# Kernel tuning notes

Measured on AMD Instinct MI355X. Metric: run time of the kernel, lower is better.

## Reference

```python
import jax, jax.numpy as jnp
import numpy as np
from jax import lax

B, L, H, I, Z = 1024, 128, 256, 32, 128  # batch, max_length, hidden, input_size, latent


def setup_inputs() -> dict:
    key = jax.random.key(0)
    ks = jax.random.split(key, 32)
    p = lambda k, shape: (jax.random.normal(k, shape, dtype=jnp.float32) * 0.05)
    d = {
        "x": jax.random.normal(ks[0], (B, Z), dtype=jnp.float32),
        "W1": p(ks[1], (512, Z)), "b1": p(ks[2], (512,)),
        "W2": p(ks[3], (512, 512)), "b2": p(ks[4], (512,)),
        "W3": p(ks[5], (512, 512)), "b3": p(ks[6], (512,)),
        # predict_h / predict_c / predict_x_0 heads
        "Wh1": p(ks[7], (512, 512)), "bh1": p(ks[8], (512,)),
        "Wh2": p(ks[9], (H, 512)), "bh2": p(ks[10], (H,)),
        "Wc1": p(ks[11], (512, 512)), "bc1": p(ks[12], (512,)),
        "Wc2": p(ks[13], (H, 512)), "bc2": p(ks[14], (H,)),
        "Wx1": p(ks[15], (512, 512)), "bx1": p(ks[16], (512,)),
        "Wx2": p(ks[17], (H, 512)), "bx2": p(ks[18], (H,)),
        # decode LSTM (input H -> hidden H), PyTorch gate order i,f,g,o
        "rWih": p(ks[19], (4 * H, H)), "rWhh": p(ks[20], (4 * H, H)),
        "rbih": p(ks[21], (4 * H,)), "rbhh": p(ks[22], (4 * H,)),
        # predictor LSTM (input H -> hidden I)
        "pWih": p(ks[23], (4 * I, H)), "pWhh": p(ks[24], (4 * I, I)),
        "pbih": p(ks[25], (4 * I,)), "pbhh": p(ks[26], (4 * I,)),
    }
    return d


def _leaky(v):
    return jnp.where(v >= 0, v, 0.2 * v)


def _lstm_cell(xt, h, c, Wih, Whh, b):
    gates = xt @ Wih.T + h @ Whh.T + b  # [B, 4G]
    i, f, g, o = jnp.split(gates, 4, axis=-1)
    c_new = jax.nn.sigmoid(f) * c + jax.nn.sigmoid(i) * jnp.tanh(g)
    h_new = jax.nn.sigmoid(o) * jnp.tanh(c_new)
    return h_new, c_new


def _forward(x, W1, b1, W2, b2, W3, b3, Wh1, bh1, Wh2, bh2, Wc1, bc1, Wc2, bc2,
             Wx1, bx1, Wx2, bx2, rWih, rWhh, rbih, rbhh, pWih, pWhh, pbih, pbhh):
    t = _leaky(x @ W1.T + b1)
    t = _leaky(t @ W2.T + b2)
    t = _leaky(t @ W3.T + b3)
    h = _leaky(t @ Wh1.T + bh1) @ Wh2.T + bh2   # [B, H]
    c = _leaky(t @ Wc1.T + bc1) @ Wc2.T + bc2   # [B, H]
    x0 = _leaky(t @ Wx1.T + bx1) @ Wx2.T + bx2  # [B, H]

    rb = rbih + rbhh
    # The torch loop re-feeds the growing sequence through the LSTM from the
    # same initial (h, c) each step; deterministically this equals a single
    # O(L) self-feeding scan: token_{i} = h-output of step i, fed at step i+1.
    def dec_step(carry, _):
        tok, hh, cc = carry
        h2, c2 = _lstm_cell(tok, hh, cc, rWih, rWhh, rb)
        return (h2, h2, c2), h2

    _, outs = lax.scan(dec_step, (x0, h, c), None, length=L)  # [L, B, H]

    pb = pbih + pbhh
    def pred_step(carry, xt):
        hh, cc = carry
        hh, cc = _lstm_cell(xt, hh, cc, pWih, pWhh, pb)
        return (hh, cc), hh

    h0 = jnp.zeros((B, I), dtype=x.dtype)
    _, pouts = lax.scan(pred_step, (h0, h0), outs)  # [L, B, I]
    y = jnp.transpose(pouts, (1, 0, 2))  # [B, L, I]

    layer_type = jax.nn.softmax(y[..., : I - 1], axis=-1)
    features = jax.nn.sigmoid(y[..., I - 1:])
    return jnp.concatenate([layer_type, features], axis=-1)


def reference(x, W1, b1, W2, b2, W3, b3, Wh1, bh1, Wh2, bh2, Wc1, bc1, Wc2, bc2,
              Wx1, bx1, Wx2, bx2, rWih, rWhh, rbih, rbhh, pWih, pWhh, pbih, pbhh):
    return _forward(x, W1, b1, W2, b2, W3, b3, Wh1, bh1, Wh2, bh2, Wc1, bc1, Wc2, bc2,
                    Wx1, bx1, Wx2, bx2, rWih, rWhh, rbih, rbhh, pWih, pWhh, pbih, pbhh)
```

## Files before the change

kernel.cpp:

```cpp
#include <hip/hip_runtime.h>
#include <hip/hip_fp8.h>

typedef unsigned short u16;
typedef unsigned char u8;
typedef __attribute__((ext_vector_type(8))) __bf16 bfrag;
typedef long long f8frag;
typedef __attribute__((ext_vector_type(4))) float f32x4;

static __device__ __forceinline__ f32x4 MFMA(bfrag a, bfrag b, f32x4 c) {
  return __builtin_amdgcn_mfma_f32_16x16x32_bf16(a, b, c, 0, 0, 0);
}
static __device__ __forceinline__ f32x4 MFMA8(f8frag a, f8frag b, f32x4 c) {
  return __builtin_amdgcn_mfma_f32_16x16x32_fp8_fp8(a, b, c, 0, 0, 0);
}

static __device__ __forceinline__ u16 f2b(float f) {
  union { float f; unsigned u; } v; v.f = f;
  unsigned r = (v.u + 0x7fffu + ((v.u >> 16) & 1u)) >> 16;
  return (u16)r;
}
static __device__ __forceinline__ u8 f2e4m3(float f) {
  return (u8)(__builtin_amdgcn_cvt_pk_fp8_f32(f, f, 0, false) & 0xff);
}
static __device__ __forceinline__ unsigned pk4_e4m3(float a, float b, float c, float d) {
  int p = __builtin_amdgcn_cvt_pk_fp8_f32(a, b, 0, false);
  p = __builtin_amdgcn_cvt_pk_fp8_f32(c, d, p, true);
  return (unsigned)p;
}
static __device__ __forceinline__ float rcp(float x) { return __builtin_amdgcn_rcpf(x); }
static __device__ __forceinline__ float ssig(float x) {
  float E = __expf(x);
  return E * rcp(1.f + E);
}
static __device__ __forceinline__ float stanh(float x) {
  float E = __expf(2.f * x);
  return 1.f - 2.f * rcp(E + 1.f);
}
static __device__ __forceinline__ float2 lstm2(float gi, float gf, float gg,
                                               float go, float c) {
  float Ei = __expf(gi), Ef = __expf(gf), Eg = __expf(2.f * gg), Eo = __expf(go);
  float P = 1.f + Ef, Q = 1.f + Ei, R = 1.f + Eg;
  float QR = Q * R;
  float num = c * Ef * QR + Ei * P * (Eg - 1.f);
  float cn = num * rcp(P * QR);
  float Ec = __expf(2.f * cn);
  float hn = Eo * (Ec - 1.f) * rcp((1.f + Eo) * (Ec + 1.f));
  return make_float2(hn, cn);
}

#define LDS_BARRIER() asm volatile("s_waitcnt lgkmcnt(0)\ns_barrier" ::: "memory")
#define PIN_A8(A) asm volatile("" : "+a"(A[0]), "+a"(A[1]), "+a"(A[2]), "+a"(A[3]), \
                                    "+a"(A[4]), "+a"(A[5]), "+a"(A[6]), "+a"(A[7]))
#define PIN_V8(A) asm volatile("" : "+v"(A[0]), "+v"(A[1]), "+v"(A[2]), "+v"(A[3]), \
                                    "+v"(A[4]), "+v"(A[5]), "+v"(A[6]), "+v"(A[7]))

struct PrepArgs {
  const float *x, *W1, *W2, *W3, *Wh1, *Wc1, *Wx1, *Wh2, *Wc2, *Wx2;
  const float *rWih, *rWhh, *rbih, *rbhh, *pWih, *pWhh, *pbih, *pbhh;
  u16 *Xbf, *W1b, *W2b, *W3b, *Wh1b, *Wc1b, *Wx1b, *Wh2b, *Wc2b, *Wx2b;
  u16 *WcatR;
  u8 *WsS, *pWsS, *pWhhS;
  float *rbR, *pbR;
};

static __device__ __forceinline__ void emit_stream(u16* dst, const float* src,
                                                   int i, int K, int ktbits) {
  int j = i & 7, lane = (i >> 3) & 63;
  int kt = (i >> 9) & ((1 << ktbits) - 1);
  int nt = (i >> (9 + ktbits)) & 3;
  int ct = i >> (11 + ktbits);
  int srow = ct * 64 + nt * 16 + (lane & 15);
  int scol = kt * 32 + ((lane >> 4) & 3) * 8 + j;
  dst[i] = f2b(src[srow * K + scol]);
}

__global__ __launch_bounds__(256) void prep(PrepArgs p) {
  const int tid0 = blockIdx.x * 256 + threadIdx.x;
  const int stride = gridDim.x * 256;
  switch (blockIdx.y) {
    case 0: for (int i = tid0; i < 131072; i += stride) p.Xbf[i] = f2b(p.x[i]); break;
    case 1: for (int i = tid0; i < 65536;  i += stride) emit_stream(p.W1b, p.W1, i, 128, 2); break;
    case 2: for (int i = tid0; i < 262144; i += stride) emit_stream(p.W2b, p.W2, i, 512, 4); break;
    case 3: for (int i = tid0; i < 262144; i += stride) emit_stream(p.W3b, p.W3, i, 512, 4); break;
    case 4: for (int i = tid0; i < 262144; i += stride) emit_stream(p.Wh1b, p.Wh1, i, 512, 4); break;
    case 5: for (int i = tid0; i < 262144; i += stride) emit_stream(p.Wc1b, p.Wc1, i, 512, 4); break;
    case 6: for (int i = tid0; i < 262144; i += stride) emit_stream(p.Wx1b, p.Wx1, i, 512, 4); break;
    case 7: for (int i = tid0; i < 131072; i += stride) emit_stream(p.Wh2b, p.Wh2, i, 512, 4); break;
    case 8: for (int i = tid0; i < 131072; i += stride) emit_stream(p.Wc2b, p.Wc2, i, 512, 4); break;
    case 9: for (int i = tid0; i < 131072; i += stride) emit_stream(p.Wx2b, p.Wx2, i, 512, 4); break;
    case 10:
      for (int i = tid0; i < 262144; i += stride) {
        int n = i >> 8, k = i & 255;
        int srow = (((n >> 4) & 3) << 8) + ((n >> 6) << 4) + (n & 15);
        p.WcatR[n * 512 + k] = f2b(p.rWih[srow * 256 + k]);
        p.WcatR[n * 512 + 256 + k] = f2b(p.rWhh[srow * 256 + k]);
      }
      break;
    case 11:
      for (int i = tid0; i < 1024; i += stride) {
        int srow = (((i >> 4) & 3) << 8) + ((i >> 6) << 4) + (i & 15);
        p.rbR[i] = p.rbih[srow] + p.rbhh[srow];
      }
      break;
    case 12:
      for (int i = tid0; i < 32768; i += stride) {
        int j = i & 7, lane = (i >> 3) & 63, kt = (i >> 9) & 7, w = i >> 12;
        int n = w * 16 + (lane & 15);
        int srow = ((n & 3) << 5) + (n >> 2);
        int k = kt * 32 + ((lane >> 4) & 3) * 8 + j;
        p.pWsS[i] = f2e4m3(p.pWih[srow * 256 + k]);
      }
      break;
    case 13:
      for (int i = tid0; i < 4096; i += stride) {
        int j = i & 7, lane = (i >> 3) & 63, w = i >> 9;
        int n = w * 16 + (lane & 15);
        int srow = ((n & 3) << 5) + (n >> 2);
        int k = ((lane >> 4) & 3) * 8 + j;
        p.pWhhS[i] = f2e4m3(p.pWhh[srow * 32 + k]);
      }
      break;
    case 14:
      for (int i = tid0; i < 128; i += stride) {
        int srow = ((i & 3) << 5) + (i >> 2);
        p.pbR[i] = p.pbih[srow] + p.pbhh[srow];
      }
      break;
    case 15:
      for (int i = tid0; i < 262144; i += stride) {
        int j = i & 7, lane = (i >> 3) & 63, kt = (i >> 9) & 7;
        int gate = (i >> 12) & 3, g16 = i >> 14;
        int srow = gate * 256 + g16 * 16 + (lane & 15);
        int k = kt * 32 + ((lane >> 4) & 3) * 8 + j;
        p.WsS[i] = f2e4m3(p.rWih[srow * 256 + k] + p.rWhh[srow * 256 + k]);
      }
      break;
  }
}

__global__ __launch_bounds__(256) void gemm_act(
    const u16* __restrict__ X, const u16* __restrict__ W,
    const float* __restrict__ bias,
    u16* __restrict__ Yb, float* __restrict__ Yf,
    int K, int ldo, int coloff, int leaky) {
  const int rt = blockIdx.x, ct = blockIdx.y;
  const int lane = threadIdx.x & 63, wave = threadIdx.x >> 6;
  const int m15 = lane & 15, q = lane >> 4, kq = q * 8;
  const int KT = K >> 5;
  const int row = rt * 64 + wave * 16 + m15;
  f32x4 acc[4] = {};
  const u16* xp = X + (size_t)row * K + kq;
  const u16* wst = W + lane * 8;
  for (int kt = 0; kt < KT; kt++) {
    bfrag a = *(const bfrag*)(xp + kt * 32);
#pragma unroll
    for (int nt = 0; nt < 4; nt++) {
      const u16* wp = wst + (size_t)((ct * 4 + nt) * KT + kt) * 512;
      acc[nt] = MFMA(a, *(const bfrag*)wp, acc[nt]);
    }
  }
#pragma unroll
  for (int nt = 0; nt < 4; nt++) {
    int col = ct * 64 + nt * 16 + m15;
    float bv = bias[col];
#pragma unroll
    for (int r = 0; r < 4; r++) {
      int orow = rt * 64 + wave * 16 + q * 4 + r;
      float v = acc[nt][r] + bv;
      if (leaky) v = v >= 0.f ? v : 0.2f * v;
      if (Yb) Yb[(size_t)orow * ldo + coloff + col] = f2b(v);
      else    Yf[(size_t)orow * ldo + coloff + col] = v;
    }
  }
}

__global__ __launch_bounds__(256) void decode_step(
    const u16* __restrict__ A, const u16* __restrict__ W,
    const float* __restrict__ rb,
    float* __restrict__ C, u16* __restrict__ Hout, int K) {
  __shared__ float g[64][128];
  const int rt = blockIdx.x, cg = blockIdx.y;
  const int lane = threadIdx.x & 63, wave = threadIdx.x >> 6;
  const int m15 = lane & 15, q = lane >> 4, kq = q * 8;
  const int row = rt * 64 + wave * 16 + m15;
  f32x4 acc[8] = {};
  const u16* ap = A + (size_t)row * K + kq;
  for (int k0 = 0; k0 < K; k0 += 32) {
    bfrag a = *(const bfrag*)(ap + k0);
#pragma unroll
    for (int nt = 0; nt < 8; nt++) {
      const u16* wp = W + (size_t)(cg * 128 + nt * 16 + m15) * K + k0 + kq;
      acc[nt] = MFMA(a, *(const bfrag*)wp, acc[nt]);
    }
  }
#pragma unroll
  for (int nt = 0; nt < 8; nt++)
#pragma unroll
    for (int r = 0; r < 4; r++)
      g[wave * 16 + q * 4 + r][nt * 16 + m15] = acc[nt][r];
  __syncthreads();
  for (int t = threadIdx.x; t < 2048; t += 256) {
    int rl = t >> 5, hc = t & 31;
    int grow = rt * 64 + rl, gcol = cg * 32 + hc;
    int base = ((hc >> 4) << 6) + (hc & 15);
    float gi = g[rl][base +  0] + rb[cg * 128 + base +  0];
    float gf = g[rl][base + 16] + rb[cg * 128 + base + 16];
    float gg = g[rl][base + 32] + rb[cg * 128 + base + 32];
    float go = g[rl][base + 48] + rb[cg * 128 + base + 48];
    size_t ci = (size_t)grow * 256 + gcol;
    float c = C[ci];
    float2 hc2 = lstm2(gi, gf, gg, go, c);
    C[ci] = hc2.y;
    Hout[ci] = f2b(hc2.x);
  }
}

__global__ __attribute__((amdgpu_flat_work_group_size(1024, 1024), amdgpu_waves_per_eu(4, 4)))
void decode_h(
    const u8* __restrict__ WsS,
    const float* __restrict__ rb,
    const float* __restrict__ C0,
    const u16* __restrict__ H0,
    u8* __restrict__ hG) {
  __shared__ __align__(16) u8 hbufS[2][4096];
  __shared__ __align__(16) u8 WoL[16][4096];
  const int tid = threadIdx.x;
  const int w = tid >> 6, lane = tid & 63;
  const int m15 = lane & 15, q = lane >> 4;
  const int b = blockIdx.x;
  const int rowg = b * 16;

  {
    int4* dst = (int4*)WoL;
    for (int i = tid; i < 4096; i += 1024) {
      int wv = i >> 8, rest = i & 255;
      dst[i] = ((const int4*)(WsS + wv * 16384 + 12288))[rest];
    }
  }
  {
    int r = tid >> 6, c = (tid & 63) * 4;
    const u16* src = H0 + (size_t)(rowg + r) * 256 + c;
    float f0, f1, f2, f3;
    { union { float f; unsigned u; } v; v.u = (unsigned)src[0] << 16; f0 = v.f; }
    { union { float f; unsigned u; } v; v.u = (unsigned)src[1] << 16; f1 = v.f; }
    { union { float f; unsigned u; } v; v.u = (unsigned)src[2] << 16; f2 = v.f; }
    { union { float f; unsigned u; } v; v.u = (unsigned)src[3] << 16; f3 = v.f; }
    unsigned hv = pk4_e4m3(f0, f1, f2, f3);
    int off = (c >> 5) * 512 + ((c >> 3) & 3) * 128 + r * 8 + (c & 4);
    *(unsigned*)(&hbufS[0][off]) = hv;
    *(unsigned*)(hG + (size_t)b * 524288 + off) = hv;
  }
  f32x4 cst = *(const f32x4*)(C0 + (size_t)(rowg + m15) * 256 + w * 16 + q * 4);
  const float* rbp = rb + w * 64 + q * 4;
  f32x4 rbv0 = *(const f32x4*)(rbp +  0);
  f32x4 rbv1 = *(const f32x4*)(rbp + 16);
  f32x4 rbv2 = *(const f32x4*)(rbp + 32);
  f32x4 rbv3 = *(const f32x4*)(rbp + 48);
  asm volatile("" : "+v"(rbv0), "+v"(rbv1), "+v"(rbv2), "+v"(rbv3));
  const u8* wsb = WsS + (size_t)w * 16384 + lane * 8;
  f8frag Wv0[8], Wv1[8], Wv2[8];
#pragma unroll
  for (int kt = 0; kt < 8; kt++) {
    Wv0[kt] = *(const f8frag*)(wsb + kt * 512);
    Wv1[kt] = *(const f8frag*)(wsb + 4096 + kt * 512);
    Wv2[kt] = *(const f8frag*)(wsb + 8192 + kt * 512);
  }
  PIN_A8(Wv0); PIN_A8(Wv1); PIN_A8(Wv2);
  const int wroff = (w >> 1) * 512 + ((w & 1) * 2 + (q >> 1)) * 128 + m15 * 8 + (q & 1) * 4;
  const u8* woW = &WoL[w][lane * 8];
  u8* hGs = hG + (size_t)b * 524288 + wroff;
  __syncthreads();

  for (int s = 1; s < 128; s++) {
    PIN_A8(Wv0); PIN_A8(Wv1); PIN_A8(Wv2);
    asm volatile("" : "+v"(rbv0), "+v"(rbv1), "+v"(rbv2), "+v"(rbv3));
    const u8* h8 = &hbufS[(s - 1) & 1][lane * 8];
    f32x4 ai = rbv0, af_ = rbv1, ag = rbv2, ao = rbv3;
#pragma unroll
    for (int kt = 0; kt < 8; kt++) {
      f8frag a8 = *(const f8frag*)(h8 + kt * 512);
      f8frag wo = *(const f8frag*)(woW + kt * 512);
      ai  = MFMA8(Wv0[kt], a8, ai);
      af_ = MFMA8(Wv1[kt], a8, af_);
      ag  = MFMA8(Wv2[kt], a8, ag);
      ao  = MFMA8(wo, a8, ao);
    }
    float hn[4];
#pragma unroll
    for (int r = 0; r < 4; r++) {
      float2 hc2 = lstm2(ai[r], af_[r], ag[r], ao[r], cst[r]);
      hn[r] = hc2.x;
      cst[r] = hc2.y;
    }
    unsigned hv = pk4_e4m3(hn[0], hn[1], hn[2], hn[3]);
    *(unsigned*)(&hbufS[s & 1][wroff]) = hv;
    *(unsigned*)(hGs + s * 4096) = hv;
    LDS_BARRIER();
  }
}

__global__ __launch_bounds__(512, 2) void pred_y(
    const u8* __restrict__ hG,
    const u8* __restrict__ pWsS,
    const u8* __restrict__ pWhhS,
    const float* __restrict__ pb,
    float* __restrict__ out) {
  __shared__ __align__(16) u8 stageL[16384];
  __shared__ __align__(16) u8 hp8[2][16][40];
  __shared__ float ysC[4][16][36];
  const int tid = threadIdx.x;
  const int w = tid >> 6, lane = tid & 63;
  const int m15 = lane & 15, q = lane >> 4;
  const int b = blockIdx.x, rowg = b * 16;
  for (int i = tid; i < 2 * 16 * 40; i += 512) (&hp8[0][0][0])[i] = 0;
  const u8* pwsb = pWsS + (size_t)w * 4096 + lane * 8;
  f8frag pbv[8];
#pragma unroll
  for (int kt = 0; kt < 8; kt++) pbv[kt] = *(const f8frag*)(pwsb + kt * 512);
  f8frag phw = *(const f8frag*)(pWhhS + (size_t)w * 512 + lane * 8);
  PIN_V8(pbv);
  asm volatile("" : "+v"(phw));
  const f32x4 pbias = *(const f32x4*)(pb + w * 16 + q * 4);
  float cp = 0.f;
  const int4* hGb = (const int4*)(hG + (size_t)b * 524288);
  const int t_si = (tid >> 3) >> 4, t_r = (tid >> 3) & 15, sub = tid & 7;
  __syncthreads();

  for (int cs = 0; cs < 32; cs++) {
    {
      int4* sdst = (int4*)stageL;
      sdst[tid] = hGb[cs * 1024 + tid];
      sdst[tid + 512] = hGb[cs * 1024 + tid + 512];
    }
    __syncthreads();
#pragma unroll
    for (int si = 0; si < 4; si++) {
      const int s = cs * 4 + si;
      const u8* xr8 = &stageL[si * 4096 + lane * 8];
      f32x4 pacc = pbias;
#pragma unroll
      for (int kt = 0; kt < 8; kt++) {
        f8frag pav = *(const f8frag*)(xr8 + kt * 512);
        pacc = MFMA8(pbv[kt], pav, pacc);
      }
      f8frag pah = *(const f8frag*)(&hp8[s & 1][m15][q * 8]);
      pacc = MFMA8(phw, pah, pacc);
      float2 hc2 = lstm2(pacc[0], pacc[1], pacc[2], pacc[3], cp);
      cp = hc2.y;
      hp8[(s + 1) & 1][m15][w * 4 + q] = f2e4m3(hc2.x);
      ysC[si][m15][w * 4 + q] = hc2.x;
      LDS_BARRIER();
    }
    {
      f32x4 yv = *(const f32x4*)&ysC[t_si][t_r][sub * 4];
      float v3 = (sub == 7) ? -1e30f : yv[3];
      float m = fmaxf(fmaxf(yv[0], yv[1]), fmaxf(yv[2], v3));
#pragma unroll
      for (int off = 4; off; off >>= 1) m = fmaxf(m, __shfl_xor(m, off, 8));
      float e0 = __expf(yv[0] - m), e1 = __expf(yv[1] - m), e2 = __expf(yv[2] - m);
      float e3 = (sub == 7) ? 0.f : __expf(yv[3] - m);
      float tot = e0 + e1 + e2 + e3;
#pragma unroll
      for (int off = 4; off; off >>= 1) tot += __shfl_xor(tot, off, 8);
      float inv = rcp(tot);
      f32x4 o;
      o[0] = e0 * inv; o[1] = e1 * inv; o[2] = e2 * inv;
      o[3] = (sub == 7) ? ssig(yv[3]) : e3 * inv;
      *(f32x4*)(out + (size_t)(rowg + t_r) * 4096 + (cs * 4 + t_si) * 32 + sub * 4) = o;
    }
    LDS_BARRIER();
  }
}

extern "C" void kernel_launch(void* const* d_in, const int* in_sizes, int n_in,
                              void* d_out, int out_size, void* d_ws, size_t ws_size,
                              hipStream_t stream) {
  (void)in_sizes; (void)n_in; (void)out_size; (void)ws_size;
  const float* x    = (const float*)d_in[0];
  const float* W1   = (const float*)d_in[1];
  const float* b1   = (const float*)d_in[2];
  const float* W2   = (const float*)d_in[3];
  const float* b2   = (const float*)d_in[4];
  const float* W3   = (const float*)d_in[5];
  const float* b3   = (const float*)d_in[6];
  const float* Wh1  = (const float*)d_in[7];
  const float* bh1  = (const float*)d_in[8];
  const float* Wh2  = (const float*)d_in[9];
  const float* bh2  = (const float*)d_in[10];
  const float* Wc1  = (const float*)d_in[11];
  const float* bc1  = (const float*)d_in[12];
  const float* Wc2  = (const float*)d_in[13];
  const float* bc2  = (const float*)d_in[14];
  const float* Wx1  = (const float*)d_in[15];
  const float* bx1  = (const float*)d_in[16];
  const float* Wx2  = (const float*)d_in[17];
  const float* bx2  = (const float*)d_in[18];
  const float* rWih = (const float*)d_in[19];
  const float* rWhh = (const float*)d_in[20];
  const float* rbih = (const float*)d_in[21];
  const float* rbhh = (const float*)d_in[22];
  const float* pWih = (const float*)d_in[23];
  const float* pWhh = (const float*)d_in[24];
  const float* pbih = (const float*)d_in[25];
  const float* pbhh = (const float*)d_in[26];

  char* w = (char*)d_ws;
  auto alloc = [&](size_t bytes) -> char* {
    char* p = w;
    w += (bytes + 255) & ~(size_t)255;
    return p;
  };
  u16* Xbf  = (u16*)alloc(1024 * 128 * 2);
  u16* T1   = (u16*)alloc(1024 * 512 * 2);
  u16* T2   = (u16*)alloc(1024 * 512 * 2);
  u16* T3   = (u16*)alloc(1024 * 512 * 2);
  u16* TH   = (u16*)alloc(1024 * 512 * 2);
  u16* TC   = (u16*)alloc(1024 * 512 * 2);
  u16* TX   = (u16*)alloc(1024 * 512 * 2);
  u16* X0H  = (u16*)alloc(1024 * 512 * 2);
  float* CB = (float*)alloc(1024 * 256 * 4);
  u16* OUTS0= (u16*)alloc(1024 * 256 * 2);
  u16* W1b  = (u16*)alloc(512 * 128 * 2);
  u16* W2b  = (u16*)alloc(512 * 512 * 2);
  u16* W3b  = (u16*)alloc(512 * 512 * 2);
  u16* Wh1b = (u16*)alloc(512 * 512 * 2);
  u16* Wc1b = (u16*)alloc(512 * 512 * 2);
  u16* Wx1b = (u16*)alloc(512 * 512 * 2);
  u16* Wh2b = (u16*)alloc(256 * 512 * 2);
  u16* Wc2b = (u16*)alloc(256 * 512 * 2);
  u16* Wx2b = (u16*)alloc(256 * 512 * 2);
  u16* WcatR= (u16*)alloc(1024 * 512 * 2);
  u8*  WsS  = (u8*)alloc(262144);
  u8*  pWsS = (u8*)alloc(32768);
  u8*  pWhhS= (u8*)alloc(4096);
  float* rbR = (float*)alloc(1024 * 4);
  float* pbR = (float*)alloc(128 * 4);
  u8*  hG   = (u8*)alloc((size_t)64 * 128 * 4096);

  PrepArgs pa;
  pa.x = x; pa.W1 = W1; pa.W2 = W2; pa.W3 = W3; pa.Wh1 = Wh1; pa.Wc1 = Wc1; pa.Wx1 = Wx1;
  pa.Wh2 = Wh2; pa.Wc2 = Wc2; pa.Wx2 = Wx2;
  pa.rWih = rWih; pa.rWhh = rWhh; pa.rbih = rbih; pa.rbhh = rbhh;
  pa.pWih = pWih; pa.pWhh = pWhh; pa.pbih = pbih; pa.pbhh = pbhh;
  pa.Xbf = Xbf; pa.W1b = W1b; pa.W2b = W2b; pa.W3b = W3b; pa.Wh1b = Wh1b;
  pa.Wc1b = Wc1b; pa.Wx1b = Wx1b; pa.Wh2b = Wh2b; pa.Wc2b = Wc2b; pa.Wx2b = Wx2b;
  pa.WcatR = WcatR;
  pa.WsS = WsS; pa.pWsS = pWsS; pa.pWhhS = pWhhS;
  pa.rbR = rbR; pa.pbR = pbR;
  prep<<<dim3(32, 16), 256, 0, stream>>>(pa);

  gemm_act<<<dim3(16, 8), 256, 0, stream>>>(Xbf, W1b, b1, T1, nullptr, 128, 512, 0, 1);
  gemm_act<<<dim3(16, 8), 256, 0, stream>>>(T1, W2b, b2, T2, nullptr, 512, 512, 0, 1);
  gemm_act<<<dim3(16, 8), 256, 0, stream>>>(T2, W3b, b3, T3, nullptr, 512, 512, 0, 1);
  gemm_act<<<dim3(16, 8), 256, 0, stream>>>(T3, Wh1b, bh1, TH, nullptr, 512, 512, 0, 1);
  gemm_act<<<dim3(16, 8), 256, 0, stream>>>(T3, Wc1b, bc1, TC, nullptr, 512, 512, 0, 1);
  gemm_act<<<dim3(16, 8), 256, 0, stream>>>(T3, Wx1b, bx1, TX, nullptr, 512, 512, 0, 1);
  gemm_act<<<dim3(16, 4), 256, 0, stream>>>(TH, Wh2b, bh2, X0H, nullptr, 512, 512, 256, 0);
  gemm_act<<<dim3(16, 4), 256, 0, stream>>>(TC, Wc2b, bc2, nullptr, CB, 512, 256, 0, 0);
  gemm_act<<<dim3(16, 4), 256, 0, stream>>>(TX, Wx2b, bx2, X0H, nullptr, 512, 512, 0, 0);

  decode_step<<<dim3(16, 8), 256, 0, stream>>>(X0H, WcatR, rbR, CB, OUTS0, 512);
  decode_h<<<64, 1024, 0, stream>>>(WsS, rbR, CB, OUTS0, hG);
  pred_y<<<64, 512, 0, stream>>>(hG, pWsS, pWhhS, pbR, (float*)d_out);
}
```

Measured before the change: 517.8 us.

## Fold first decode LSTM step into decode_h and batch head GEMMs into grouped launches

Removes the separate decode_step kernel by computing the first LSTM step (bf16 MFMA over the concatenated input/hidden weights, re-laid out in MFMA fragment order) inside decode_h, eliminating the OUTS0 round-trip and one launch. The three head GEMMs of each layer are merged into single grouped launches via blockIdx.z, cutting launch count from six to two. In exchange, each decode_h block now streams its slice of the 1 MB WcatR weights from global memory before the recurrent loop, which adds startup latency to a 64-block kernel.

```diff
diff --git a/kernel.cpp b/kernel.cpp
--- a/kernel.cpp
+++ b/kernel.cpp
@@ -31,10 +31,6 @@
 static __device__ __forceinline__ float ssig(float x) {
   float E = __expf(x);
   return E * rcp(1.f + E);
-}
-static __device__ __forceinline__ float stanh(float x) {
-  float E = __expf(2.f * x);
-  return 1.f - 2.f * rcp(E + 1.f);
 }
 static __device__ __forceinline__ float2 lstm2(float gi, float gf, float gg,
                                                float go, float c) {
@@ -89,11 +85,13 @@
     case 8: for (int i = tid0; i < 131072; i += stride) emit_stream(p.Wc2b, p.Wc2, i, 512, 4); break;
     case 9: for (int i = tid0; i < 131072; i += stride) emit_stream(p.Wx2b, p.Wx2, i, 512, 4); break;
     case 10:
-      for (int i = tid0; i < 262144; i += stride) {
-        int n = i >> 8, k = i & 255;
-        int srow = (((n >> 4) & 3) << 8) + ((n >> 6) << 4) + (n & 15);
-        p.WcatR[n * 512 + k] = f2b(p.rWih[srow * 256 + k]);
-        p.WcatR[n * 512 + 256 + k] = f2b(p.rWhh[srow * 256 + k]);
+      for (int i = tid0; i < 524288; i += stride) {
+        int j = i & 7, lane = (i >> 3) & 63, kt = (i >> 9) & 15;
+        int gate = (i >> 13) & 3, w16 = i >> 15;
+        int srow = gate * 256 + w16 * 16 + (lane & 15);
+        int k = kt * 32 + ((lane >> 4) & 3) * 8 + j;
+        float v = (k < 256) ? p.rWih[srow * 256 + k] : p.rWhh[srow * 256 + (k - 256)];
+        p.WcatR[i] = f2b(v);
       }
       break;
     case 11:
@@ -174,53 +172,53 @@
   }
 }
 
-__global__ __launch_bounds__(256) void decode_step(
-    const u16* __restrict__ A, const u16* __restrict__ W,
-    const float* __restrict__ rb,
-    float* __restrict__ C, u16* __restrict__ Hout, int K) {
-  __shared__ float g[64][128];
-  const int rt = blockIdx.x, cg = blockIdx.y;
+struct G3 {
+  const u16 *X, *W;
+  const float* bias;
+  u16* Yb;
+  float* Yf;
+  int K, ldo, coloff, leaky;
+};
+__global__ __launch_bounds__(256) void gemm_act3(G3 ga, G3 gb, G3 gc) {
+  G3 g = (blockIdx.z == 0) ? ga : (blockIdx.z == 1) ? gb : gc;
+  const int rt = blockIdx.x, ct = blockIdx.y;
   const int lane = threadIdx.x & 63, wave = threadIdx.x >> 6;
   const int m15 = lane & 15, q = lane >> 4, kq = q * 8;
+  const int KT = g.K >> 5;
   const int row = rt * 64 + wave * 16 + m15;
-  f32x4 acc[8] = {};
-  const u16* ap = A + (size_t)row * K + kq;
-  for (int k0 = 0; k0 < K; k0 += 32) {
-    bfrag a = *(const bfrag*)(ap + k0);
-#pragma unroll
-    for (int nt = 0; nt < 8; nt++) {
-      const u16* wp = W + (size_t)(cg * 128 + nt * 16 + m15) * K + k0 + kq;
+  f32x4 acc[4] = {};
+  const u16* xp = g.X + (size_t)row * g.K + kq;
+  const u16* wst = g.W + lane * 8;
+  for (int kt = 0; kt < KT; kt++) {
+    bfrag a = *(const bfrag*)(xp + kt * 32);
+#pragma unroll
+    for (int nt = 0; nt < 4; nt++) {
+      const u16* wp = wst + (size_t)((ct * 4 + nt) * KT + kt) * 512;
       acc[nt] = MFMA(a, *(const bfrag*)wp, acc[nt]);
     }
   }
 #pragma unroll
-  for (int nt = 0; nt < 8; nt++)
-#pragma unroll
-    for (int r = 0; r < 4; r++)
-      g[wave * 16 + q * 4 + r][nt * 16 + m15] = acc[nt][r];
-  __syncthreads();
-  for (int t = threadIdx.x; t < 2048; t += 256) {
-    int rl = t >> 5, hc = t & 31;
-    int grow = rt * 64 + rl, gcol = cg * 32 + hc;
-    int base = ((hc >> 4) << 6) + (hc & 15);
-    float gi = g[rl][base +  0] + rb[cg * 128 + base +  0];
-    float gf = g[rl][base + 16] + rb[cg * 128 + base + 16];
-    float gg = g[rl][base + 32] + rb[cg * 128 + base + 32];
-    float go = g[rl][base + 48] + rb[cg * 128 + base + 48];
-    size_t ci = (size_t)grow * 256 + gcol;
-    float c = C[ci];
-    float2 hc2 = lstm2(gi, gf, gg, go, c);
-    C[ci] = hc2.y;
-    Hout[ci] = f2b(hc2.x);
+  for (int nt = 0; nt < 4; nt++) {
+    int col = ct * 64 + nt * 16 + m15;
+    float bv = g.bias[col];
+#pragma unroll
+    for (int r = 0; r < 4; r++) {
+      int orow = rt * 64 + wave * 16 + q * 4 + r;
+      float v = acc[nt][r] + bv;
+      if (g.leaky) v = v >= 0.f ? v : 0.2f * v;
+      if (g.Yb) g.Yb[(size_t)orow * g.ldo + g.coloff + col] = f2b(v);
+      else      g.Yf[(size_t)orow * g.ldo + g.coloff + col] = v;
+    }
   }
 }
 
 __global__ __attribute__((amdgpu_flat_work_group_size(1024, 1024), amdgpu_waves_per_eu(4, 4)))
 void decode_h(
     const u8* __restrict__ WsS,
+    const u16* __restrict__ WcatR,
     const float* __restrict__ rb,
-    const float* __restrict__ C0,
-    const u16* __restrict__ H0,
+    const float* __restrict__ CB,
+    const u16* __restrict__ X0H,
     u8* __restrict__ hG) {
   __shared__ __align__(16) u8 hbufS[2][4096];
   __shared__ __align__(16) u8 WoL[16][4096];
@@ -237,26 +235,39 @@
       dst[i] = ((const int4*)(WsS + wv * 16384 + 12288))[rest];
     }
   }
-  {
-    int r = tid >> 6, c = (tid & 63) * 4;
-    const u16* src = H0 + (size_t)(rowg + r) * 256 + c;
-    float f0, f1, f2, f3;
-    { union { float f; unsigned u; } v; v.u = (unsigned)src[0] << 16; f0 = v.f; }
-    { union { float f; unsigned u; } v; v.u = (unsigned)src[1] << 16; f1 = v.f; }
-    { union { float f; unsigned u; } v; v.u = (unsigned)src[2] << 16; f2 = v.f; }
-    { union { float f; unsigned u; } v; v.u = (unsigned)src[3] << 16; f3 = v.f; }
-    unsigned hv = pk4_e4m3(f0, f1, f2, f3);
-    int off = (c >> 5) * 512 + ((c >> 3) & 3) * 128 + r * 8 + (c & 4);
-    *(unsigned*)(&hbufS[0][off]) = hv;
-    *(unsigned*)(hG + (size_t)b * 524288 + off) = hv;
-  }
-  f32x4 cst = *(const f32x4*)(C0 + (size_t)(rowg + m15) * 256 + w * 16 + q * 4);
   const float* rbp = rb + w * 64 + q * 4;
   f32x4 rbv0 = *(const f32x4*)(rbp +  0);
   f32x4 rbv1 = *(const f32x4*)(rbp + 16);
   f32x4 rbv2 = *(const f32x4*)(rbp + 32);
   f32x4 rbv3 = *(const f32x4*)(rbp + 48);
   asm volatile("" : "+v"(rbv0), "+v"(rbv1), "+v"(rbv2), "+v"(rbv3));
+  f32x4 cst = *(const f32x4*)(CB + (size_t)(rowg + m15) * 256 + w * 16 + q * 4);
+  const int wroff = (w >> 1) * 512 + ((w & 1) * 2 + (q >> 1)) * 128 + m15 * 8 + (q & 1) * 4;
+  u8* hGs = hG + (size_t)b * 524288 + wroff;
+
+  {
+    f32x4 ai = rbv0, af_ = rbv1, ag = rbv2, ao = rbv3;
+    const u16* xrow = X0H + (size_t)(rowg + m15) * 512 + q * 8;
+    const u16* wcw = WcatR + (size_t)w * 32768 + lane * 8;
+#pragma unroll
+    for (int kt = 0; kt < 16; kt++) {
+      bfrag a = *(const bfrag*)(xrow + kt * 32);
+      ai  = MFMA(*(const bfrag*)(wcw + kt * 512), a, ai);
+      af_ = MFMA(*(const bfrag*)(wcw + 8192 + kt * 512), a, af_);
+      ag  = MFMA(*(const bfrag*)(wcw + 16384 + kt * 512), a, ag);
+      ao  = MFMA(*(const bfrag*)(wcw + 24576 + kt * 512), a, ao);
+    }
+    float hn[4];
+#pragma unroll
+    for (int r = 0; r < 4; r++) {
+      float2 hc2 = lstm2(ai[r], af_[r], ag[r], ao[r], cst[r]);
+      hn[r] = hc2.x;
+      cst[r] = hc2.y;
+    }
+    unsigned hv = pk4_e4m3(hn[0], hn[1], hn[2], hn[3]);
+    *(unsigned*)(&hbufS[0][wroff]) = hv;
+    *(unsigned*)hGs = hv;
+  }
   const u8* wsb = WsS + (size_t)w * 16384 + lane * 8;
   f8frag Wv0[8], Wv1[8], Wv2[8];
 #pragma unroll
@@ -266,9 +277,7 @@
     Wv2[kt] = *(const f8frag*)(wsb + 8192 + kt * 512);
   }
   PIN_A8(Wv0); PIN_A8(Wv1); PIN_A8(Wv2);
-  const int wroff = (w >> 1) * 512 + ((w & 1) * 2 + (q >> 1)) * 128 + m15 * 8 + (q & 1) * 4;
   const u8* woW = &WoL[w][lane * 8];
-  u8* hGs = hG + (size_t)b * 524288 + wroff;
   __syncthreads();
 
   for (int s = 1; s < 128; s++) {
@@ -294,7 +303,7 @@
     }
     unsigned hv = pk4_e4m3(hn[0], hn[1], hn[2], hn[3]);
     *(unsigned*)(&hbufS[s & 1][wroff]) = hv;
-    *(unsigned*)(hGs + s * 4096) = hv;
+    *(unsigned*)(hGs + (size_t)s * 4096) = hv;
     LDS_BARRIER();
   }
 }
@@ -419,7 +428,6 @@
   u16* TX   = (u16*)alloc(1024 * 512 * 2);
   u16* X0H  = (u16*)alloc(1024 * 512 * 2);
   float* CB = (float*)alloc(1024 * 256 * 4);
-  u16* OUTS0= (u16*)alloc(1024 * 256 * 2);
   u16* W1b  = (u16*)alloc(512 * 128 * 2);
   u16* W2b  = (u16*)alloc(512 * 512 * 2);
   u16* W3b  = (u16*)alloc(512 * 512 * 2);
@@ -452,14 +460,15 @@
   gemm_act<<<dim3(16, 8), 256, 0, stream>>>(Xbf, W1b, b1, T1, nullptr, 128, 512, 0, 1);
   gemm_act<<<dim3(16, 8), 256, 0, stream>>>(T1, W2b, b2, T2, nullptr, 512, 512, 0, 1);
   gemm_act<<<dim3(16, 8), 256, 0, stream>>>(T2, W3b, b3, T3, nullptr, 512, 512, 0, 1);
-  gemm_act<<<dim3(16, 8), 256, 0, stream>>>(T3, Wh1b, bh1, TH, nullptr, 512, 512, 0, 1);
-  gemm_act<<<dim3(16, 8), 256, 0, stream>>>(T3, Wc1b, bc1, TC, nullptr, 512, 512, 0, 1);
-  gemm_act<<<dim3(16, 8), 256, 0, stream>>>(T3, Wx1b, bx1, TX, nullptr, 512, 512, 0, 1);
-  gemm_act<<<dim3(16, 4), 256, 0, stream>>>(TH, Wh2b, bh2, X0H, nullptr, 512, 512, 256, 0);
-  gemm_act<<<dim3(16, 4), 256, 0, stream>>>(TC, Wc2b, bc2, nullptr, CB, 512, 256, 0, 0);
-  gemm_act<<<dim3(16, 4), 256, 0, stream>>>(TX, Wx2b, bx2, X0H, nullptr, 512, 512, 0, 0);
-
-  decode_step<<<dim3(16, 8), 256, 0, stream>>>(X0H, WcatR, rbR, CB, OUTS0, 512);
-  decode_h<<<64, 1024, 0, stream>>>(WsS, rbR, CB, OUTS0, hG);
+  G3 h1a = {T3, Wh1b, bh1, TH, nullptr, 512, 512, 0, 1};
+  G3 h1b = {T3, Wc1b, bc1, TC, nullptr, 512, 512, 0, 1};
+  G3 h1c = {T3, Wx1b, bx1, TX, nullptr, 512, 512, 0, 1};
+  gemm_act3<<<dim3(16, 8, 3), 256, 0, stream>>>(h1a, h1b, h1c);
+  G3 h2a = {TH, Wh2b, bh2, X0H, nullptr, 512, 512, 256, 0};
+  G3 h2b = {TC, Wc2b, bc2, nullptr, CB, 512, 256, 0, 0};
+  G3 h2c = {TX, Wx2b, bx2, X0H, nullptr, 512, 512, 0, 0};
+  gemm_act3<<<dim3(16, 4, 3), 256, 0, stream>>>(h2a, h2b, h2c);
+
+  decode_h<<<64, 1024, 0, stream>>>(WsS, WcatR, rbR, CB, X0H, hG);
   pred_y<<<64, 512, 0, stream>>>(hG, pWsS, pWhhS, pbR, (float*)d_out);
 }
```

Measured after the change: 487.3 us. -5.9%, faster.
